# Kernel tuning notes

Hardware: AMD Instinct MI355X
Metric: run time of the kernel (lower is better)

## Reference

```python
import jax, jax.numpy as jnp
import numpy as np

N_HEAD = 16


def setup_inputs() -> dict:
    key = jax.random.key(0)
    k1, k2, k3 = jax.random.split(key, 3)
    B, T, C = 2, 2048, 1024
    x = jax.random.normal(k1, (B, T, C), dtype=jnp.float32)
    w_attn = jax.random.normal(k2, (C, 3 * C), dtype=jnp.float32) * 0.02
    w_proj = jax.random.normal(k3, (C, C), dtype=jnp.float32) * 0.02
    return {"x": x, "w_attn": w_attn, "w_proj": w_proj}


def reference(x, w_attn, w_proj):
    B, T, C = x.shape
    H = N_HEAD
    D = C // H
    qkv = x @ w_attn  # [B, T, 3C]
    q, k, v = jnp.split(qkv, 3, axis=2)
    q = q.reshape(B, T, H, D)
    k = k.reshape(B, T, H, D)
    v = v.reshape(B, T, H, D)
    scale = 1.0 / jnp.sqrt(jnp.asarray(D, dtype=x.dtype))
    # Full T x T score matrix, matching the 'standard_attention' path.
    att = jnp.einsum('bthd,bshd->bhts', q, k) * scale  # [B, H, T, T]
    causal = jnp.tril(jnp.ones((T, T), dtype=bool))
    att = jnp.where(causal[None, None, :, :], att, jnp.asarray(-jnp.inf, dtype=att.dtype))
    att = jax.nn.softmax(att, axis=-1)
    # dropout_p is False (== 0.0) in the original module, so no dropout applied.
    y = jnp.einsum('bhts,bshd->bthd', att, v)  # [B, T, H, D]
    y = y.reshape(B, T, C)
    return y @ w_proj
```

## Files before the change

### kernel.cpp

```cpp
#include <hip/hip_runtime.h>
#include <hip/hip_bf16.h>
#include <math.h>

#define BB 2
#define TT 2048
#define HH 16
#define DD 64
#define CC 1024
#define C3 3072

typedef __attribute__((ext_vector_type(8))) short bf16x8;
typedef __attribute__((ext_vector_type(4))) short bf16x4;
typedef __attribute__((ext_vector_type(4))) float f32x4;
typedef __attribute__((ext_vector_type(2))) unsigned int u32x2;

__device__ __forceinline__ unsigned short f2bf(float f) {
  union { float f; unsigned u; } v; v.f = f;
  unsigned r = v.u + 0x7fffu + ((v.u >> 16) & 1u);
  return (unsigned short)(r >> 16);
}
__device__ __forceinline__ unsigned pack2bf(float a, float b) {
  __hip_bfloat162 h = __float22bfloat162_rn(make_float2(a, b));
  union { __hip_bfloat162 h; unsigned u; } cv; cv.h = h;
  return cv.u;
}

__device__ __forceinline__ void async_cp16(const void* g, void* l) {
  __builtin_amdgcn_global_load_lds(
      (const __attribute__((address_space(1))) void*)g,
      (__attribute__((address_space(3))) void*)l, 16, 0, 0);
}

__global__ __launch_bounds__(256)
void prep(const float* __restrict__ x, const float* __restrict__ w_attn,
          const float* __restrict__ w_proj, unsigned short* __restrict__ xb,
          unsigned short* __restrict__ wat, unsigned short* __restrict__ wpt) {
  __shared__ __align__(16) float Ts[64][68];
  const int bx = blockIdx.x, tid = threadIdx.x;
  if (bx < 1024) {
    int i = bx * 256 + tid;
#pragma unroll
    for (int it = 0; it < 4; ++it, i += 262144) {
      const float4 v = ((const float4*)x)[i];
      bf16x4 o = {(short)f2bf(v.x), (short)f2bf(v.y),
                  (short)f2bf(v.z), (short)f2bf(v.w)};
      ((bf16x4*)xb)[i] = o;
    }
    return;
  }
  const float* W;
  unsigned short* WT;
  int Nd, bound, n0, k0;
  float s;
  if (bx < 1792) {
    const int bid = bx - 1024;
    W = w_attn; WT = wat; Nd = 3072; bound = 1024; s = 0.18033688f;
    n0 = (bid % 48) * 64; k0 = (bid / 48) * 64;
  } else {
    const int bid = bx - 1792;
    W = w_proj; WT = wpt; Nd = 1024; bound = 0; s = 1.0f;
    n0 = (bid % 16) * 64; k0 = (bid / 16) * 64;
  }
  const int rl = tid >> 4, c4 = tid & 15;
#pragma unroll
  for (int it = 0; it < 4; ++it) {
    const int r = it * 16 + rl;
    *(float4*)&Ts[r][c4 * 4] =
        *(const float4*)(W + (size_t)(k0 + r) * Nd + n0 + c4 * 4);
  }
  __syncthreads();
#pragma unroll
  for (int it = 0; it < 4; ++it) {
    const int n = it * 16 + rl;
    const float sc = (n0 + n < bound) ? s : 1.0f;
    bf16x4 o = {(short)f2bf(Ts[c4 * 4 + 0][n] * sc),
                (short)f2bf(Ts[c4 * 4 + 1][n] * sc),
                (short)f2bf(Ts[c4 * 4 + 2][n] * sc),
                (short)f2bf(Ts[c4 * 4 + 3][n] * sc)};
    *(bf16x4*)(WT + (size_t)(n0 + n) * CC + k0 + c4 * 4) = o;
  }
}

__global__ __launch_bounds__(256, 3)
void gemm_qkv(const unsigned short* __restrict__ A,
              const unsigned short* __restrict__ BT,
              unsigned short* __restrict__ Cb,
              unsigned short* __restrict__ Vout) {
  __shared__ __align__(16) unsigned short As[2 * 128 * 32];
  __shared__ __align__(16) unsigned short Bs[2 * 128 * 32];

  const int tid = threadIdx.x;
  const int w = tid >> 6, lane = tid & 63;
  const int l15 = lane & 15, quad = lane >> 4;
  const int wm = w >> 1, wn = w & 1;
  const int row0 = blockIdx.y * 128, col0 = blockIdx.x * 128;

  const int ca0 = tid, ca1 = tid + 256;
  const int ra0 = ca0 >> 2, ka0 = ((ca0 & 3) ^ ((ca0 >> 3) & 3)) * 8;
  const int ra1 = ca1 >> 2, ka1 = ((ca1 & 3) ^ ((ca1 >> 3) & 3)) * 8;
  const unsigned short* gA0 = A + (size_t)(row0 + ra0) * CC + ka0;
  const unsigned short* gA1 = A + (size_t)(row0 + ra1) * CC + ka1;
  const unsigned short* gB0 = BT + (size_t)(col0 + ra0) * CC + ka0;
  const unsigned short* gB1 = BT + (size_t)(col0 + ra1) * CC + ka1;
  const int la0 = tid * 16, la1 = tid * 16 + 4096;

  const int fro = l15 * 64 + 16 * (quad ^ ((l15 >> 1) & 3));

  f32x4 acc[4][4];
#pragma unroll
  for (int i = 0; i < 4; ++i)
#pragma unroll
    for (int j = 0; j < 4; ++j) acc[i][j] = (f32x4){0.f, 0.f, 0.f, 0.f};

  async_cp16(gA0, (char*)As + la0);
  async_cp16(gA1, (char*)As + la1);
  async_cp16(gB0, (char*)Bs + la0);
  async_cp16(gB1, (char*)Bs + la1);

  for (int i = 0; i < 32; ++i) {
    const int cur = i & 1;
    __syncthreads();

    if (i + 1 < 32) {
      const int k1 = (i + 1) * 32;
      const int ab = (cur ^ 1) * 8192;
      async_cp16(gA0 + k1, (char*)As + ab + la0);
      async_cp16(gA1 + k1, (char*)As + ab + la1);
      async_cp16(gB0 + k1, (char*)Bs + ab + la0);
      async_cp16(gB1 + k1, (char*)Bs + ab + la1);
    }

    const char* fA = (const char*)As + cur * 8192 + wm * 4096 + fro;
    const char* fB = (const char*)Bs + cur * 8192 + wn * 4096 + fro;

    bf16x8 af[4], bf[4];
#pragma unroll
    for (int mt = 0; mt < 4; ++mt) af[mt] = *(const bf16x8*)(fA + mt * 1024);
#pragma unroll
    for (int nt = 0; nt < 4; ++nt) bf[nt] = *(const bf16x8*)(fB + nt * 1024);
#pragma unroll
    for (int mt = 0; mt < 4; ++mt)
#pragma unroll
      for (int nt = 0; nt < 4; ++nt)
        acc[mt][nt] = __builtin_amdgcn_mfma_f32_16x16x32_bf16(
            af[mt], bf[nt], acc[mt][nt], 0, 0, 0);
  }

  if (col0 >= 2048) {
#pragma unroll
    for (int mt = 0; mt < 4; ++mt) {
      const int rbase = row0 + wm * 64 + mt * 16 + quad * 4;
      const int bq = rbase >> 11, t0 = rbase & 2047;
#pragma unroll
      for (int nt = 0; nt < 4; ++nt) {
        const int d = col0 + wn * 64 + nt * 16 + l15 - 2048;
        bf16x4 o = {(short)f2bf(acc[mt][nt][0]), (short)f2bf(acc[mt][nt][1]),
                    (short)f2bf(acc[mt][nt][2]), (short)f2bf(acc[mt][nt][3])};
        *(bf16x4*)(Vout + (((size_t)(bq << 10) + d) << 11) + t0) = o;
      }
    }
  } else {
#pragma unroll
    for (int mt = 0; mt < 4; ++mt) {
      const int rbase = row0 + wm * 64 + mt * 16 + quad * 4;
#pragma unroll
      for (int r = 0; r < 4; ++r) {
        unsigned short* cr =
            Cb + (size_t)(rbase + r) * C3 + col0 + wn * 64 + l15;
#pragma unroll
        for (int nt = 0; nt < 4; ++nt) cr[nt * 16] = f2bf(acc[mt][nt][r]);
      }
    }
  }
}

__global__ __launch_bounds__(256, 2)
void gemm_out(const unsigned short* __restrict__ A,
              const unsigned short* __restrict__ BT,
              float* __restrict__ Cf) {
  __shared__ __align__(16) unsigned short As[2 * 64 * 64];
  __shared__ __align__(16) unsigned short Bs[2 * 128 * 64];

  const int tid = threadIdx.x;
  const int w = tid >> 6, lane = tid & 63;
  const int l15 = lane & 15, quad = lane >> 4;
  const int wm = w >> 1, wn = w & 1;
  const int row0 = blockIdx.y * 64, col0 = blockIdx.x * 128;

  const int ca0 = tid, ca1 = tid + 256;
  const int ra0 = ca0 >> 3, ka0 = ((ca0 & 7) ^ ((ca0 >> 3) & 7)) * 8;
  const int ra1 = ca1 >> 3, ka1 = ((ca1 & 7) ^ ((ca1 >> 3) & 7)) * 8;
  const unsigned short* gA0 = A + (size_t)(row0 + ra0) * CC + ka0;
  const unsigned short* gA1 = A + (size_t)(row0 + ra1) * CC + ka1;
  const unsigned short* gB[4];
  int lb[4];
#pragma unroll
  for (int t = 0; t < 4; ++t) {
    const int c = tid + t * 256;
    const int rb = c >> 3, kb = ((c & 7) ^ ((c >> 3) & 7)) * 8;
    gB[t] = BT + (size_t)(col0 + rb) * CC + kb;
    lb[t] = c * 16;
  }
  const int la0 = tid * 16, la1 = tid * 16 + 4096;

  const int fro = l15 * 128 + ((quad ^ (l15 & 7)) << 4);

  f32x4 acc[2][4];
#pragma unroll
  for (int i = 0; i < 2; ++i)
#pragma unroll
    for (int j = 0; j < 4; ++j) acc[i][j] = (f32x4){0.f, 0.f, 0.f, 0.f};

  async_cp16(gA0, (char*)As + la0);
  async_cp16(gA1, (char*)As + la1);
#pragma unroll
  for (int t = 0; t < 4; ++t) async_cp16(gB[t], (char*)Bs + lb[t]);

  for (int i = 0; i < 16; ++i) {
    const int cur = i & 1;
    __syncthreads();

    if (i + 1 < 16) {
      const int k1 = (i + 1) * 64;
      const int ab = (cur ^ 1) * 8192, bb = (cur ^ 1) * 16384;
      async_cp16(gA0 + k1, (char*)As + ab + la0);
      async_cp16(gA1 + k1, (char*)As + ab + la1);
#pragma unroll
      for (int t = 0; t < 4; ++t) async_cp16(gB[t] + k1, (char*)Bs + bb + lb[t]);
    }

    const char* fA = (const char*)As + cur * 8192 + wm * 4096 + fro;
    const char* fB = (const char*)Bs + cur * 16384 + wn * 8192 + fro;

#pragma unroll
    for (int kh = 0; kh < 2; ++kh) {
      const int xo = kh * 64;
      bf16x8 af[2], bf[4];
#pragma unroll
      for (int mt = 0; mt < 2; ++mt)
        af[mt] = *(const bf16x8*)(fA + mt * 2048 + ((fro + xo) & 127) - (fro & 127));
#pragma unroll
      for (int nt = 0; nt < 4; ++nt)
        bf[nt] = *(const bf16x8*)(fB + nt * 2048 + ((fro + xo) & 127) - (fro & 127));
#pragma unroll
      for (int mt = 0; mt < 2; ++mt)
#pragma unroll
        for (int nt = 0; nt < 4; ++nt)
          acc[mt][nt] = __builtin_amdgcn_mfma_f32_16x16x32_bf16(
              af[mt], bf[nt], acc[mt][nt], 0, 0, 0);
    }
  }

#pragma unroll
  for (int mt = 0; mt < 2; ++mt) {
    const int rbase = row0 + wm * 32 + mt * 16 + quad * 4;
#pragma unroll
    for (int r = 0; r < 4; ++r) {
      float* cr = Cf + (size_t)(rbase + r) * CC + col0 + wn * 64 + l15;
#pragma unroll
      for (int nt = 0; nt < 4; ++nt) cr[nt * 16] = acc[mt][nt][r];
    }
  }
}

__global__ __launch_bounds__(512, 4)
void attn_mfma(const unsigned short* __restrict__ qkvb,
               const unsigned short* __restrict__ vt,
               unsigned short* __restrict__ y) {
  const int n = blockIdx.x;
  const int bh = (n & 7) + 8 * ((n >> 3) & 3);
  const int m = n >> 5;
  const int qb = (m < 8) ? m : 23 - m;
  const int b = bh >> 4, h = bh & 15;
  const int tid = threadIdx.x;
  const int w = tid >> 6;
  const int lane = tid & 63;
  const int l15 = lane & 15, quad = lane >> 4;

  __shared__ __align__(16) char Kb[2 * 8192];
  __shared__ __align__(16) char Vb[2 * 8192];
  __shared__ __align__(16) unsigned short Ps[8 * 16 * 72];

  char* psw = (char*)Ps + w * 2304;
  const int psrow = l15 * 144;

  const int lr = lane >> 3;
  const int lc = lane & 7;
  const int srcoff = ((lc ^ lr) << 4);
  const char* ksrc = (const char*)qkvb + ((size_t)(b * TT) * C3 + 1024 + h * 64) * 2;
  const char* vsrc = (const char*)vt + ((size_t)(b * HH + h) * DD * TT) * 2;

  const int fro = l15 * 128 + ((quad ^ (l15 & 7)) << 4);

  bf16x8 onesf;
#pragma unroll
  for (int jj = 0; jj < 8; ++jj) onesf[jj] = (short)0x3F80;

  const int nt = 2 * qb + 2;
  const int qrow_my = qb * 128 + w * 16 + l15;
  const int jlast = (qb * 128 + w * 16 + 15) >> 6;

  const unsigned short* qrow =
      qkvb + (size_t)(b * TT + qb * 128 + w * 16 + l15) * C3 + h * DD;
  bf16x8 qf0 = *(const bf16x8*)(qrow + quad * 8);
  bf16x8 qf1 = *(const bf16x8*)(qrow + 32 + quad * 8);

  f32x4 O[4];
#pragma unroll
  for (int dt = 0; dt < 4; ++dt) O[dt] = (f32x4){0.f, 0.f, 0.f, 0.f};
  f32x4 lacc = (f32x4){0.f, 0.f, 0.f, 0.f};

  async_cp16(ksrc + (size_t)(w * 8 + lr) * (C3 * 2) + srcoff, Kb + w * 1024);
  async_cp16(vsrc + (size_t)(w * 8 + lr) * (TT * 2) + srcoff, Vb + w * 1024);

  for (int j = 0; j < nt; ++j) {
    const int cur = j & 1;
    __syncthreads();

    if (j + 1 < nt) {
      const int key1 = (j + 1) * 64;
      async_cp16(ksrc + (size_t)(key1 + w * 8 + lr) * (C3 * 2) + srcoff,
                 Kb + (cur ^ 1) * 8192 + w * 1024);
      async_cp16(vsrc + (size_t)(w * 8 + lr) * (TT * 2) + key1 * 2 + srcoff,
                 Vb + (cur ^ 1) * 8192 + w * 1024);
    }

    if (j > jlast) continue;

    const char* Kc = Kb + cur * 8192;
    const char* Vc = Vb + cur * 8192;

    f32x4 S[4];
#pragma unroll
    for (int ct = 0; ct < 4; ++ct) {
      bf16x8 k0 = *(const bf16x8*)(Kc + ct * 2048 + fro);
      bf16x8 k1 = *(const bf16x8*)(Kc + ct * 2048 + (fro ^ 64));
      f32x4 z = (f32x4){-12.f, -12.f, -12.f, -12.f};
      z = __builtin_amdgcn_mfma_f32_16x16x32_bf16(k0, qf0, z, 0, 0, 0);
      z = __builtin_amdgcn_mfma_f32_16x16x32_bf16(k1, qf1, z, 0, 0, 0);
      S[ct] = z;
    }

    if (j == jlast) {
#pragma unroll
      for (int ct = 0; ct < 4; ++ct)
#pragma unroll
        for (int r = 0; r < 4; ++r)
          if (64 * j + 16 * ct + quad * 4 + r > qrow_my) S[ct][r] = -INFINITY;
    }

#pragma unroll
    for (int ct = 0; ct < 4; ++ct) {
      u32x2 d;
      d[0] = pack2bf(__builtin_amdgcn_exp2f(S[ct][0]),
                     __builtin_amdgcn_exp2f(S[ct][1]));
      d[1] = pack2bf(__builtin_amdgcn_exp2f(S[ct][2]),
                     __builtin_amdgcn_exp2f(S[ct][3]));
      *(u32x2*)(psw + psrow + (((ct + l15) & 3) << 5) + quad * 8) = d;
    }

    bf16x8 pf0, pf1;
    {
      const int c0 = (quad >> 1), c1 = 2 + (quad >> 1);
      pf0 = *(const bf16x8*)(psw + psrow + (((c0 + l15) & 3) << 5) + ((quad & 1) << 4));
      pf1 = *(const bf16x8*)(psw + psrow + (((c1 + l15) & 3) << 5) + ((quad & 1) << 4));
    }

    lacc = __builtin_amdgcn_mfma_f32_16x16x32_bf16(onesf, pf0, lacc, 0, 0, 0);
    lacc = __builtin_amdgcn_mfma_f32_16x16x32_bf16(onesf, pf1, lacc, 0, 0, 0);
#pragma unroll
    for (int dt = 0; dt < 4; ++dt) {
      bf16x8 v0 = *(const bf16x8*)(Vc + dt * 2048 + fro);
      bf16x8 v1 = *(const bf16x8*)(Vc + dt * 2048 + (fro ^ 64));
      O[dt] = __builtin_amdgcn_mfma_f32_16x16x32_bf16(v0, pf0, O[dt], 0, 0, 0);
      O[dt] = __builtin_amdgcn_mfma_f32_16x16x32_bf16(v1, pf1, O[dt], 0, 0, 0);
    }
  }

  const float inv = 1.0f / lacc[0];
  unsigned short* yr =
      y + (size_t)(b * TT + qb * 128 + w * 16 + l15) * CC + h * DD + quad * 4;
#pragma unroll
  for (int dt = 0; dt < 4; ++dt) {
    bf16x4 o = {(short)f2bf(O[dt][0] * inv), (short)f2bf(O[dt][1] * inv),
                (short)f2bf(O[dt][2] * inv), (short)f2bf(O[dt][3] * inv)};
    *(bf16x4*)(yr + dt * 16) = o;
  }
}

extern "C" void kernel_launch(void* const* d_in, const int* in_sizes, int n_in,
                              void* d_out, int out_size, void* d_ws,
                              size_t ws_size, hipStream_t stream) {
  const float* x      = (const float*)d_in[0];
  const float* w_attn = (const float*)d_in[1];
  const float* w_proj = (const float*)d_in[2];
  float* out = (float*)d_out;

  unsigned short* xb   = (unsigned short*)d_ws;
  unsigned short* wat  = xb + (size_t)4096 * 1024;
  unsigned short* wpt  = wat + (size_t)3072 * 1024;
  unsigned short* qkvb = wpt + (size_t)1024 * 1024;
  unsigned short* vt   = qkvb + (size_t)4096 * 3072;
  unsigned short* yb   = vt + (size_t)BB * HH * DD * TT;

  dim3 blk(256);

  prep<<<2048, blk, 0, stream>>>(x, w_attn, w_proj, xb, wat, wpt);

  gemm_qkv<<<dim3(C3 / 128, (BB * TT) / 128), blk, 0, stream>>>(
      xb, wat, qkvb, vt);

  attn_mfma<<<dim3(512, 1, 1), dim3(512), 0, stream>>>(qkvb, vt, yb);

  gemm_out<<<dim3(CC / 128, (BB * TT) / 64), blk, 0, stream>>>(yb, wpt, out);
}
```

Measured before the change: 170.8 us.

## Split key tiles across wave pairs with 32-row query tiles and LDS reduction

```diff
diff --git a/kernel.cpp b/kernel.cpp
--- a/kernel.cpp
+++ b/kernel.cpp
@@ -276,12 +276,14 @@
   const int w = tid >> 6;
   const int lane = tid & 63;
   const int l15 = lane & 15, quad = lane >> 4;
+  const int wq = w >> 1, kh2 = w & 1;
 
   __shared__ __align__(16) char Kb[2 * 8192];
   __shared__ __align__(16) char Vb[2 * 8192];
-  __shared__ __align__(16) unsigned short Ps[8 * 16 * 72];
-
-  char* psw = (char*)Ps + w * 2304;
+  __shared__ __align__(16) char PsArena[8 * 4608];
+  __shared__ float Red2[4][2][16];
+
+  char* psw = PsArena + w * 4608;
   const int psrow = l15 * 144;
 
   const int lr = lane >> 3;
@@ -291,24 +293,33 @@
   const char* vsrc = (const char*)vt + ((size_t)(b * HH + h) * DD * TT) * 2;
 
   const int fro = l15 * 128 + ((quad ^ (l15 & 7)) << 4);
+  const int vxor = kh2 << 6;
 
   bf16x8 onesf;
 #pragma unroll
   for (int jj = 0; jj < 8; ++jj) onesf[jj] = (short)0x3F80;
 
   const int nt = 2 * qb + 2;
-  const int qrow_my = qb * 128 + w * 16 + l15;
-  const int jlast = (qb * 128 + w * 16 + 15) >> 6;
+  const int rmin = qb * 128 + wq * 32;
+  const int rmax = rmin + 31;
 
   const unsigned short* qrow =
-      qkvb + (size_t)(b * TT + qb * 128 + w * 16 + l15) * C3 + h * DD;
-  bf16x8 qf0 = *(const bf16x8*)(qrow + quad * 8);
-  bf16x8 qf1 = *(const bf16x8*)(qrow + 32 + quad * 8);
-
-  f32x4 O[4];
-#pragma unroll
-  for (int dt = 0; dt < 4; ++dt) O[dt] = (f32x4){0.f, 0.f, 0.f, 0.f};
-  f32x4 lacc = (f32x4){0.f, 0.f, 0.f, 0.f};
+      qkvb + (size_t)(b * TT + rmin + l15) * C3 + h * DD;
+  bf16x8 qf[2][2];
+#pragma unroll
+  for (int qg = 0; qg < 2; ++qg)
+#pragma unroll
+    for (int kh = 0; kh < 2; ++kh)
+      qf[qg][kh] = *(const bf16x8*)(qrow + qg * 16 * C3 + kh * 32 + quad * 8);
+
+  f32x4 O[4][2];
+  f32x4 lacc[2];
+#pragma unroll
+  for (int dt = 0; dt < 4; ++dt)
+#pragma unroll
+    for (int qg = 0; qg < 2; ++qg) O[dt][qg] = (f32x4){0.f, 0.f, 0.f, 0.f};
+#pragma unroll
+  for (int qg = 0; qg < 2; ++qg) lacc[qg] = (f32x4){0.f, 0.f, 0.f, 0.f};
 
   async_cp16(ksrc + (size_t)(w * 8 + lr) * (C3 * 2) + srcoff, Kb + w * 1024);
   async_cp16(vsrc + (size_t)(w * 8 + lr) * (TT * 2) + srcoff, Vb + w * 1024);
@@ -325,66 +336,105 @@
                  Vb + (cur ^ 1) * 8192 + w * 1024);
     }
 
-    if (j > jlast) continue;
+    const int klo = 64 * j + kh2 * 32;
+    if (klo > rmax) continue;
 
     const char* Kc = Kb + cur * 8192;
     const char* Vc = Vb + cur * 8192;
 
-    f32x4 S[4];
-#pragma unroll
-    for (int ct = 0; ct < 4; ++ct) {
+    f32x4 S[2][2];
+#pragma unroll
+    for (int kt = 0; kt < 2; ++kt) {
+      const int ct = kh2 * 2 + kt;
       bf16x8 k0 = *(const bf16x8*)(Kc + ct * 2048 + fro);
       bf16x8 k1 = *(const bf16x8*)(Kc + ct * 2048 + (fro ^ 64));
-      f32x4 z = (f32x4){-12.f, -12.f, -12.f, -12.f};
-      z = __builtin_amdgcn_mfma_f32_16x16x32_bf16(k0, qf0, z, 0, 0, 0);
-      z = __builtin_amdgcn_mfma_f32_16x16x32_bf16(k1, qf1, z, 0, 0, 0);
-      S[ct] = z;
-    }
-
-    if (j == jlast) {
-#pragma unroll
-      for (int ct = 0; ct < 4; ++ct)
-#pragma unroll
-        for (int r = 0; r < 4; ++r)
-          if (64 * j + 16 * ct + quad * 4 + r > qrow_my) S[ct][r] = -INFINITY;
-    }
-
-#pragma unroll
-    for (int ct = 0; ct < 4; ++ct) {
-      u32x2 d;
-      d[0] = pack2bf(__builtin_amdgcn_exp2f(S[ct][0]),
-                     __builtin_amdgcn_exp2f(S[ct][1]));
-      d[1] = pack2bf(__builtin_amdgcn_exp2f(S[ct][2]),
-                     __builtin_amdgcn_exp2f(S[ct][3]));
-      *(u32x2*)(psw + psrow + (((ct + l15) & 3) << 5) + quad * 8) = d;
-    }
-
-    bf16x8 pf0, pf1;
-    {
-      const int c0 = (quad >> 1), c1 = 2 + (quad >> 1);
-      pf0 = *(const bf16x8*)(psw + psrow + (((c0 + l15) & 3) << 5) + ((quad & 1) << 4));
-      pf1 = *(const bf16x8*)(psw + psrow + (((c1 + l15) & 3) << 5) + ((quad & 1) << 4));
-    }
-
-    lacc = __builtin_amdgcn_mfma_f32_16x16x32_bf16(onesf, pf0, lacc, 0, 0, 0);
-    lacc = __builtin_amdgcn_mfma_f32_16x16x32_bf16(onesf, pf1, lacc, 0, 0, 0);
+#pragma unroll
+      for (int qg = 0; qg < 2; ++qg) {
+        f32x4 z = (f32x4){-12.f, -12.f, -12.f, -12.f};
+        z = __builtin_amdgcn_mfma_f32_16x16x32_bf16(k0, qf[qg][0], z, 0, 0, 0);
+        z = __builtin_amdgcn_mfma_f32_16x16x32_bf16(k1, qf[qg][1], z, 0, 0, 0);
+        S[kt][qg] = z;
+      }
+    }
+
+    if (klo + 31 > rmin) {
+#pragma unroll
+      for (int kt = 0; kt < 2; ++kt)
+#pragma unroll
+        for (int qg = 0; qg < 2; ++qg)
+#pragma unroll
+          for (int r = 0; r < 4; ++r)
+            if (klo + kt * 16 + quad * 4 + r > rmin + qg * 16 + l15)
+              S[kt][qg][r] = -INFINITY;
+    }
+
+#pragma unroll
+    for (int kt = 0; kt < 2; ++kt)
+#pragma unroll
+      for (int qg = 0; qg < 2; ++qg) {
+        u32x2 d;
+        d[0] = pack2bf(__builtin_amdgcn_exp2f(S[kt][qg][0]),
+                       __builtin_amdgcn_exp2f(S[kt][qg][1]));
+        d[1] = pack2bf(__builtin_amdgcn_exp2f(S[kt][qg][2]),
+                       __builtin_amdgcn_exp2f(S[kt][qg][3]));
+        *(u32x2*)(psw + qg * 2304 + psrow + (((kt + l15) & 3) << 5) + quad * 8) = d;
+      }
+
+    bf16x8 pf[2];
+#pragma unroll
+    for (int qg = 0; qg < 2; ++qg)
+      pf[qg] = *(const bf16x8*)(psw + qg * 2304 + psrow +
+                                ((((quad >> 1) + l15) & 3) << 5) +
+                                ((quad & 1) << 4));
+
+#pragma unroll
+    for (int qg = 0; qg < 2; ++qg)
+      lacc[qg] = __builtin_amdgcn_mfma_f32_16x16x32_bf16(onesf, pf[qg], lacc[qg], 0, 0, 0);
 #pragma unroll
     for (int dt = 0; dt < 4; ++dt) {
-      bf16x8 v0 = *(const bf16x8*)(Vc + dt * 2048 + fro);
-      bf16x8 v1 = *(const bf16x8*)(Vc + dt * 2048 + (fro ^ 64));
-      O[dt] = __builtin_amdgcn_mfma_f32_16x16x32_bf16(v0, pf0, O[dt], 0, 0, 0);
-      O[dt] = __builtin_amdgcn_mfma_f32_16x16x32_bf16(v1, pf1, O[dt], 0, 0, 0);
-    }
-  }
-
-  const float inv = 1.0f / lacc[0];
-  unsigned short* yr =
-      y + (size_t)(b * TT + qb * 128 + w * 16 + l15) * CC + h * DD + quad * 4;
-#pragma unroll
-  for (int dt = 0; dt < 4; ++dt) {
-    bf16x4 o = {(short)f2bf(O[dt][0] * inv), (short)f2bf(O[dt][1] * inv),
-                (short)f2bf(O[dt][2] * inv), (short)f2bf(O[dt][3] * inv)};
-    *(bf16x4*)(yr + dt * 16) = o;
+      bf16x8 vf = *(const bf16x8*)(Vc + dt * 2048 + (fro ^ vxor));
+#pragma unroll
+      for (int qg = 0; qg < 2; ++qg)
+        O[dt][qg] = __builtin_amdgcn_mfma_f32_16x16x32_bf16(vf, pf[qg], O[dt][qg], 0, 0, 0);
+    }
+  }
+
+  const int epoff = l15 * 64 + ((quad ^ (l15 & 3)) << 4);
+  __syncthreads();
+  if (kh2) {
+    char* rs = PsArena + wq * 8192;
+#pragma unroll
+    for (int dt = 0; dt < 4; ++dt)
+#pragma unroll
+      for (int qg = 0; qg < 2; ++qg)
+        *(f32x4*)(rs + (dt * 2 + qg) * 1024 + epoff) = O[dt][qg];
+    if (quad == 0) {
+#pragma unroll
+      for (int qg = 0; qg < 2; ++qg) Red2[wq][qg][l15] = lacc[qg][0];
+    }
+  }
+  __syncthreads();
+  if (!kh2) {
+    const char* rs = PsArena + wq * 8192;
+#pragma unroll
+    for (int dt = 0; dt < 4; ++dt)
+#pragma unroll
+      for (int qg = 0; qg < 2; ++qg)
+        O[dt][qg] += *(const f32x4*)(rs + (dt * 2 + qg) * 1024 + epoff);
+    unsigned short* yr =
+        y + (size_t)(b * TT + rmin + l15) * CC + h * DD + quad * 4;
+#pragma unroll
+    for (int qg = 0; qg < 2; ++qg) {
+      const float inv = 1.0f / (lacc[qg][0] + Red2[wq][qg][l15]);
+#pragma unroll
+      for (int dt = 0; dt < 4; ++dt) {
+        bf16x4 o = {(short)f2bf(O[dt][qg][0] * inv),
+                    (short)f2bf(O[dt][qg][1] * inv),
+                    (short)f2bf(O[dt][qg][2] * inv),
+                    (short)f2bf(O[dt][qg][3] * inv)};
+        *(bf16x4*)(yr + (size_t)qg * 16 * CC + dt * 16) = o;
+      }
+    }
   }
 }
 
```

Result: no change. 174.0 us (+1.9%).

## Split attention key tiles across warp pairs with paired 64-row query tiles

Applied to the files above, without the earlier changes.

```diff
diff --git a/kernel.cpp b/kernel.cpp
--- a/kernel.cpp
+++ b/kernel.cpp
@@ -269,19 +269,20 @@
                unsigned short* __restrict__ y) {
   const int n = blockIdx.x;
   const int bh = (n & 7) + 8 * ((n >> 3) & 3);
-  const int m = n >> 5;
-  const int qb = (m < 8) ? m : 23 - m;
+  const int qp = n >> 5;
   const int b = bh >> 4, h = bh & 15;
   const int tid = threadIdx.x;
   const int w = tid >> 6;
   const int lane = tid & 63;
   const int l15 = lane & 15, quad = lane >> 4;
+  const int wq = w >> 1, kh2 = w & 1;
 
   __shared__ __align__(16) char Kb[2 * 8192];
   __shared__ __align__(16) char Vb[2 * 8192];
-  __shared__ __align__(16) unsigned short Ps[8 * 16 * 72];
-
-  char* psw = (char*)Ps + w * 2304;
+  __shared__ __align__(16) char PsArena[8 * 2304];
+  __shared__ float Red2[4][16];
+
+  char* psw = PsArena + w * 2304;
   const int psrow = l15 * 144;
 
   const int lr = lane >> 3;
@@ -291,100 +292,121 @@
   const char* vsrc = (const char*)vt + ((size_t)(b * HH + h) * DD * TT) * 2;
 
   const int fro = l15 * 128 + ((quad ^ (l15 & 7)) << 4);
-
-  bf16x8 onesf;
-#pragma unroll
-  for (int jj = 0; jj < 8; ++jj) onesf[jj] = (short)0x3F80;
-
-  const int nt = 2 * qb + 2;
-  const int qrow_my = qb * 128 + w * 16 + l15;
-  const int jlast = (qb * 128 + w * 16 + 15) >> 6;
-
-  const unsigned short* qrow =
-      qkvb + (size_t)(b * TT + qb * 128 + w * 16 + l15) * C3 + h * DD;
-  bf16x8 qf0 = *(const bf16x8*)(qrow + quad * 8);
-  bf16x8 qf1 = *(const bf16x8*)(qrow + 32 + quad * 8);
-
-  f32x4 O[4];
-#pragma unroll
-  for (int dt = 0; dt < 4; ++dt) O[dt] = (f32x4){0.f, 0.f, 0.f, 0.f};
-  f32x4 lacc = (f32x4){0.f, 0.f, 0.f, 0.f};
-
-  async_cp16(ksrc + (size_t)(w * 8 + lr) * (C3 * 2) + srcoff, Kb + w * 1024);
-  async_cp16(vsrc + (size_t)(w * 8 + lr) * (TT * 2) + srcoff, Vb + w * 1024);
-
-  for (int j = 0; j < nt; ++j) {
-    const int cur = j & 1;
+  const int vxor = kh2 << 6;
+  const int pfoff = ((((quad >> 1) + l15) & 3) << 5) + ((quad & 1) << 4);
+  const int epoff = l15 * 64 + ((quad ^ (l15 & 3)) << 4);
+
+  for (int phase = 0; phase < 2; ++phase) {
+    const int qt = phase ? qp : 31 - qp;
+    const int nt = qt + 1;
+    const int rmin = qt * 64 + wq * 16;
+    const int rmax = rmin + 15;
+    const int dk = rmax - kh2 * 32;
+    const int jl = (dk >= 0) ? (dk >> 6) : -1;
+
+    if (phase) __syncthreads();
+
+    const unsigned short* qrow =
+        qkvb + (size_t)(b * TT + rmin + l15) * C3 + h * DD;
+    bf16x8 qf0 = *(const bf16x8*)(qrow + quad * 8);
+    bf16x8 qf1 = *(const bf16x8*)(qrow + 32 + quad * 8);
+
+    f32x4 O[4];
+    float lsum = 0.f;
+#pragma unroll
+    for (int dt = 0; dt < 4; ++dt) O[dt] = (f32x4){0.f, 0.f, 0.f, 0.f};
+
+    async_cp16(ksrc + (size_t)(w * 8 + lr) * (C3 * 2) + srcoff, Kb + w * 1024);
+    async_cp16(vsrc + (size_t)(w * 8 + lr) * (TT * 2) + srcoff, Vb + w * 1024);
+
+    for (int j = 0; j < nt; ++j) {
+      const int cur = j & 1;
+      __syncthreads();
+
+      if (j + 1 < nt) {
+        const int key1 = (j + 1) * 64;
+        async_cp16(ksrc + (size_t)(key1 + w * 8 + lr) * (C3 * 2) + srcoff,
+                   Kb + (cur ^ 1) * 8192 + w * 1024);
+        async_cp16(vsrc + (size_t)(w * 8 + lr) * (TT * 2) + key1 * 2 + srcoff,
+                   Vb + (cur ^ 1) * 8192 + w * 1024);
+      }
+
+      if (j > jl) continue;
+
+      const char* Kc = Kb + cur * 8192;
+      const char* Vc = Vb + cur * 8192;
+      const int klo = 64 * j + kh2 * 32;
+
+      f32x4 S[2];
+#pragma unroll
+      for (int kt = 0; kt < 2; ++kt) {
+        const int ct = kh2 * 2 + kt;
+        bf16x8 k0 = *(const bf16x8*)(Kc + ct * 2048 + fro);
+        bf16x8 k1 = *(const bf16x8*)(Kc + ct * 2048 + (fro ^ 64));
+        f32x4 z = (f32x4){-12.f, -12.f, -12.f, -12.f};
+        z = __builtin_amdgcn_mfma_f32_16x16x32_bf16(k0, qf0, z, 0, 0, 0);
+        z = __builtin_amdgcn_mfma_f32_16x16x32_bf16(k1, qf1, z, 0, 0, 0);
+        S[kt] = z;
+      }
+
+      if (klo + 31 > rmin) {
+#pragma unroll
+        for (int kt = 0; kt < 2; ++kt)
+#pragma unroll
+          for (int r = 0; r < 4; ++r)
+            if (klo + kt * 16 + quad * 4 + r > rmin + l15)
+              S[kt][r] = -INFINITY;
+      }
+
+#pragma unroll
+      for (int kt = 0; kt < 2; ++kt) {
+        u32x2 d;
+        d[0] = pack2bf(__builtin_amdgcn_exp2f(S[kt][0]),
+                       __builtin_amdgcn_exp2f(S[kt][1]));
+        d[1] = pack2bf(__builtin_amdgcn_exp2f(S[kt][2]),
+                       __builtin_amdgcn_exp2f(S[kt][3]));
+        lsum += __uint_as_float(d[0] << 16) +
+                __uint_as_float(d[0] & 0xffff0000u) +
+                __uint_as_float(d[1] << 16) +
+                __uint_as_float(d[1] & 0xffff0000u);
+        *(u32x2*)(psw + psrow + (((kt + l15) & 3) << 5) + quad * 8) = d;
+      }
+
+      const bf16x8 pf = *(const bf16x8*)(psw + psrow + pfoff);
+#pragma unroll
+      for (int dt = 0; dt < 4; ++dt) {
+        bf16x8 vf = *(const bf16x8*)(Vc + dt * 2048 + (fro ^ vxor));
+        O[dt] = __builtin_amdgcn_mfma_f32_16x16x32_bf16(vf, pf, O[dt], 0, 0, 0);
+      }
+    }
+
+    lsum += __shfl_xor(lsum, 16, 64);
+    lsum += __shfl_xor(lsum, 32, 64);
+
     __syncthreads();
-
-    if (j + 1 < nt) {
-      const int key1 = (j + 1) * 64;
-      async_cp16(ksrc + (size_t)(key1 + w * 8 + lr) * (C3 * 2) + srcoff,
-                 Kb + (cur ^ 1) * 8192 + w * 1024);
-      async_cp16(vsrc + (size_t)(w * 8 + lr) * (TT * 2) + key1 * 2 + srcoff,
-                 Vb + (cur ^ 1) * 8192 + w * 1024);
-    }
-
-    if (j > jlast) continue;
-
-    const char* Kc = Kb + cur * 8192;
-    const char* Vc = Vb + cur * 8192;
-
-    f32x4 S[4];
-#pragma unroll
-    for (int ct = 0; ct < 4; ++ct) {
-      bf16x8 k0 = *(const bf16x8*)(Kc + ct * 2048 + fro);
-      bf16x8 k1 = *(const bf16x8*)(Kc + ct * 2048 + (fro ^ 64));
-      f32x4 z = (f32x4){-12.f, -12.f, -12.f, -12.f};
-      z = __builtin_amdgcn_mfma_f32_16x16x32_bf16(k0, qf0, z, 0, 0, 0);
-      z = __builtin_amdgcn_mfma_f32_16x16x32_bf16(k1, qf1, z, 0, 0, 0);
-      S[ct] = z;
-    }
-
-    if (j == jlast) {
-#pragma unroll
-      for (int ct = 0; ct < 4; ++ct)
-#pragma unroll
-        for (int r = 0; r < 4; ++r)
-          if (64 * j + 16 * ct + quad * 4 + r > qrow_my) S[ct][r] = -INFINITY;
-    }
-
-#pragma unroll
-    for (int ct = 0; ct < 4; ++ct) {
-      u32x2 d;
-      d[0] = pack2bf(__builtin_amdgcn_exp2f(S[ct][0]),
-                     __builtin_amdgcn_exp2f(S[ct][1]));
-      d[1] = pack2bf(__builtin_amdgcn_exp2f(S[ct][2]),
-                     __builtin_amdgcn_exp2f(S[ct][3]));
-      *(u32x2*)(psw + psrow + (((ct + l15) & 3) << 5) + quad * 8) = d;
-    }
-
-    bf16x8 pf0, pf1;
-    {
-      const int c0 = (quad >> 1), c1 = 2 + (quad >> 1);
-      pf0 = *(const bf16x8*)(psw + psrow + (((c0 + l15) & 3) << 5) + ((quad & 1) << 4));
-      pf1 = *(const bf16x8*)(psw + psrow + (((c1 + l15) & 3) << 5) + ((quad & 1) << 4));
-    }
-
-    lacc = __builtin_amdgcn_mfma_f32_16x16x32_bf16(onesf, pf0, lacc, 0, 0, 0);
-    lacc = __builtin_amdgcn_mfma_f32_16x16x32_bf16(onesf, pf1, lacc, 0, 0, 0);
-#pragma unroll
-    for (int dt = 0; dt < 4; ++dt) {
-      bf16x8 v0 = *(const bf16x8*)(Vc + dt * 2048 + fro);
-      bf16x8 v1 = *(const bf16x8*)(Vc + dt * 2048 + (fro ^ 64));
-      O[dt] = __builtin_amdgcn_mfma_f32_16x16x32_bf16(v0, pf0, O[dt], 0, 0, 0);
-      O[dt] = __builtin_amdgcn_mfma_f32_16x16x32_bf16(v1, pf1, O[dt], 0, 0, 0);
-    }
-  }
-
-  const float inv = 1.0f / lacc[0];
-  unsigned short* yr =
-      y + (size_t)(b * TT + qb * 128 + w * 16 + l15) * CC + h * DD + quad * 4;
-#pragma unroll
-  for (int dt = 0; dt < 4; ++dt) {
-    bf16x4 o = {(short)f2bf(O[dt][0] * inv), (short)f2bf(O[dt][1] * inv),
-                (short)f2bf(O[dt][2] * inv), (short)f2bf(O[dt][3] * inv)};
-    *(bf16x4*)(yr + dt * 16) = o;
+    if (kh2) {
+      char* rs = PsArena + wq * 4096;
+#pragma unroll
+      for (int dt = 0; dt < 4; ++dt)
+        *(f32x4*)(rs + dt * 1024 + epoff) = O[dt];
+      if (quad == 0) Red2[wq][l15] = lsum;
+    }
+    __syncthreads();
+    if (!kh2) {
+      const char* rs = PsArena + wq * 4096;
+#pragma unroll
+      for (int dt = 0; dt < 4; ++dt)
+        O[dt] += *(const f32x4*)(rs + dt * 1024 + epoff);
+      const float inv = 1.0f / (lsum + Red2[wq][l15]);
+      unsigned short* yr =
+          y + (size_t)(b * TT + rmin + l15) * CC + h * DD + quad * 4;
+#pragma unroll
+      for (int dt = 0; dt < 4; ++dt) {
+        bf16x4 o = {(short)f2bf(O[dt][0] * inv), (short)f2bf(O[dt][1] * inv),
+                    (short)f2bf(O[dt][2] * inv), (short)f2bf(O[dt][3] * inv)};
+        *(bf16x4*)(yr + dt * 16) = o;
+      }
+    }
   }
 }
 
```

Result: no change. 169.4 us (-0.8%).
